# Performance work log

Measured on AMD Instinct MI355X. Metric: run time of the kernel, lower is better.

Reference implementation:

```python
import jax, jax.numpy as jnp
import numpy as np

SEQ_LEN = 512
PRED_LEN = 96
N_BINS = 5


def setup_inputs() -> dict:
    key = jax.random.key(0)
    k1, k2, k3 = jax.random.split(key, 3)
    x = jax.random.normal(k1, (64, 1024, SEQ_LEN), dtype=jnp.float32)
    # nn.Linear(seq_len, pred_len): weight (pred_len, seq_len), bias (pred_len,)
    W = jax.random.normal(k2, (PRED_LEN, SEQ_LEN), dtype=jnp.float32) / np.sqrt(SEQ_LEN)
    b = jax.random.normal(k3, (PRED_LEN,), dtype=jnp.float32) * 0.01
    return {"x": x, "W": W, "b": b}


def reference(x, W, b):
    # Exact low-pass trend: keep lowest N_BINS rfft bins, zero the rest, invert.
    X = jnp.fft.rfft(x, axis=-1)                      # (B, N, seq_len//2+1) complex
    n_freq = X.shape[-1]
    keep = (jnp.arange(n_freq) < N_BINS)              # low-pass mask
    X_low = jnp.where(keep, X, 0.0)
    trend = jnp.fft.irfft(X_low, n=SEQ_LEN, axis=-1).astype(x.dtype)  # (B, N, seq_len)
    resid = x - trend
    trend_forecast = jnp.einsum('bns,ps->bnp', trend, W) + b          # (B, N, pred_len)
    return (trend_forecast, resid)
```

## Files before the change

### kernel.cpp

```cpp
#include <hip/hip_runtime.h>

#define SEQL 512
#define PREDL 96
#define NB 9
#define WBPAD 12
#define RU 4

typedef float fvec4 __attribute__((ext_vector_type(4)));

static __device__ __constant__ double TWO_PI_OVER_S = 6.283185307179586476925286766559 / (double)SEQL;

__device__ __forceinline__ float wave_sum_bcast(float v) {
    int t;
    t = __builtin_amdgcn_update_dpp(0, __float_as_int(v), 0x111, 0xf, 0xf, true); v += __int_as_float(t);
    t = __builtin_amdgcn_update_dpp(0, __float_as_int(v), 0x112, 0xf, 0xf, true); v += __int_as_float(t);
    t = __builtin_amdgcn_update_dpp(0, __float_as_int(v), 0x114, 0xf, 0xf, true); v += __int_as_float(t);
    t = __builtin_amdgcn_update_dpp(0, __float_as_int(v), 0x118, 0xf, 0xf, true); v += __int_as_float(t);
    t = __builtin_amdgcn_update_dpp(0, __float_as_int(v), 0x142, 0xf, 0xf, true); v += __int_as_float(t);
    t = __builtin_amdgcn_update_dpp(0, __float_as_int(v), 0x143, 0xf, 0xf, true); v += __int_as_float(t);
    return __int_as_float(__builtin_amdgcn_readlane(__float_as_int(v), 63));
}

__global__ void basis_kernel(float* __restrict__ tbl) {
    int s = threadIdx.x;
    if (s >= SEQL) return;
    tbl[0 * SEQL + s] = 1.0f;
    #pragma unroll
    for (int k = 1; k <= 4; ++k) {
        double ang = TWO_PI_OVER_S * (double)(k * s);
        tbl[(2 * k - 1) * SEQL + s] = (float)cos(ang);
        tbl[(2 * k    ) * SEQL + s] = (float)sin(ang);
    }
}

__global__ __launch_bounds__(64)
void wb_kernel(const float* __restrict__ W, const float* __restrict__ tbl,
               float* __restrict__ wb) {
    int p = blockIdx.x;
    int lane = threadIdx.x;
    const float* wr = W + (size_t)p * SEQL + lane * 8;
    float4 wa = *(const float4*)(wr);
    float4 wz = *(const float4*)(wr + 4);
    float wv[8] = {wa.x, wa.y, wa.z, wa.w, wz.x, wz.y, wz.z, wz.w};
    #pragma unroll
    for (int j = 0; j < NB; ++j) {
        const float* bj = tbl + j * SEQL + lane * 8;
        float4 b0 = *(const float4*)bj;
        float4 b1 = *(const float4*)(bj + 4);
        float bb[8] = {b0.x, b0.y, b0.z, b0.w, b1.x, b1.y, b1.z, b1.w};
        float acc = 0.f;
        #pragma unroll
        for (int e = 0; e < 8; ++e) acc += wv[e] * bb[e];
        float s = wave_sum_bcast(acc);
        if (lane == 0) wb[p * WBPAD + j] = s;
    }
}

__global__ __launch_bounds__(256)
void detrend_kernel(const float* __restrict__ x, const float* __restrict__ bias,
                    const float* __restrict__ tbl, const float* __restrict__ wb,
                    float* __restrict__ fc, float* __restrict__ resid, int nrows) {
    const int lane = threadIdx.x & 63;
    const int wid  = threadIdx.x >> 6;
    const int wpb  = blockDim.x >> 6;
    const int gw   = blockIdx.x * wpb + wid;
    const int nw   = gridDim.x * wpb;

    float bas[NB][8];
    #pragma unroll
    for (int j = 0; j < NB; ++j) {
        const float* bj = tbl + j * SEQL + lane * 8;
        float4 b0 = *(const float4*)bj;
        float4 b1 = *(const float4*)(bj + 4);
        bas[j][0] = b0.x; bas[j][1] = b0.y; bas[j][2] = b0.z; bas[j][3] = b0.w;
        bas[j][4] = b1.x; bas[j][5] = b1.y; bas[j][6] = b1.z; bas[j][7] = b1.w;
    }
    const int p0 = lane;
    const int p1 = 64 + lane;
    float wb0[NB], wb1[NB], bv0, bv1 = 0.f;
    #pragma unroll
    for (int j = 0; j < NB; ++j) wb0[j] = wb[p0 * WBPAD + j];
    bv0 = bias[p0];
    if (lane < 32) {
        #pragma unroll
        for (int j = 0; j < NB; ++j) wb1[j] = wb[p1 * WBPAD + j];
        bv1 = bias[p1];
    }

    for (int r0 = gw * RU; r0 < nrows; r0 += nw * RU) {
        float xv[RU][8];
        #pragma unroll
        for (int u = 0; u < RU; ++u) {
            const float* xr = x + (size_t)(r0 + u) * SEQL + lane * 8;
            float4 xa = *(const float4*)xr;
            float4 xb = *(const float4*)(xr + 4);
            xv[u][0] = xa.x; xv[u][1] = xa.y; xv[u][2] = xa.z; xv[u][3] = xa.w;
            xv[u][4] = xb.x; xv[u][5] = xb.y; xv[u][6] = xb.z; xv[u][7] = xb.w;
        }

        float c[RU][NB];
        #pragma unroll
        for (int u = 0; u < RU; ++u) {
            float acc[NB];
            #pragma unroll
            for (int j = 0; j < NB; ++j) acc[j] = 0.f;
            #pragma unroll
            for (int e = 0; e < 8; ++e)
                #pragma unroll
                for (int j = 0; j < NB; ++j) acc[j] += xv[u][e] * bas[j][e];
            acc[0] *= (1.0f / SEQL);
            #pragma unroll
            for (int j = 1; j < NB; ++j) acc[j] *= (2.0f / SEQL);
            #pragma unroll
            for (int j = 0; j < NB; ++j) c[u][j] = wave_sum_bcast(acc[j]);
        }

        #pragma unroll
        for (int u = 0; u < RU; ++u) {
            float rv[8];
            #pragma unroll
            for (int e = 0; e < 8; ++e) {
                float t = 0.f;
                #pragma unroll
                for (int j = 0; j < NB; ++j) t += c[u][j] * bas[j][e];
                rv[e] = xv[u][e] - t;
            }
            float* rr = resid + (size_t)(r0 + u) * SEQL + lane * 8;
            fvec4 v0 = {rv[0], rv[1], rv[2], rv[3]};
            fvec4 v1 = {rv[4], rv[5], rv[6], rv[7]};
            __builtin_nontemporal_store(v0, (fvec4*)rr);
            __builtin_nontemporal_store(v1, (fvec4*)(rr + 4));
        }

        #pragma unroll
        for (int u = 0; u < RU; ++u) {
            float* fr = fc + (size_t)(r0 + u) * PREDL;
            float f0 = bv0;
            #pragma unroll
            for (int j = 0; j < NB; ++j) f0 += c[u][j] * wb0[j];
            __builtin_nontemporal_store(f0, fr + p0);
            if (lane < 32) {
                float f1 = bv1;
                #pragma unroll
                for (int j = 0; j < NB; ++j) f1 += c[u][j] * wb1[j];
                __builtin_nontemporal_store(f1, fr + p1);
            }
        }
    }
}

extern "C" void kernel_launch(void* const* d_in, const int* in_sizes, int n_in,
                              void* d_out, int out_size, void* d_ws, size_t ws_size,
                              hipStream_t stream) {
    const float* x = (const float*)d_in[0];
    const float* W = (const float*)d_in[1];
    const float* b = (const float*)d_in[2];
    float* fc = (float*)d_out;
    const int nrows = in_sizes[0] / SEQL;
    float* resid = fc + (size_t)nrows * PREDL;
    float* tbl = (float*)d_ws;
    float* wb  = tbl + NB * SEQL;

    hipLaunchKernelGGL(basis_kernel, dim3(1), dim3(SEQL), 0, stream, tbl);
    hipLaunchKernelGGL(wb_kernel, dim3(PREDL), dim3(64), 0, stream, W, tbl, wb);
    hipLaunchKernelGGL(detrend_kernel, dim3(2048), dim3(256), 0, stream,
                       x, b, tbl, wb, fc, resid, nrows);
}
```

Baseline: 64.87 us.

## Issue all row loads upfront with one tile per wave and fast basis sincos

```diff
diff --git a/kernel.cpp b/kernel.cpp
--- a/kernel.cpp
+++ b/kernel.cpp
@@ -4,11 +4,9 @@
 #define PREDL 96
 #define NB 9
 #define WBPAD 12
-#define RU 4
+#define RU 8
 
 typedef float fvec4 __attribute__((ext_vector_type(4)));
-
-static __device__ __constant__ double TWO_PI_OVER_S = 6.283185307179586476925286766559 / (double)SEQL;
 
 __device__ __forceinline__ float wave_sum_bcast(float v) {
     int t;
@@ -27,9 +25,12 @@
     tbl[0 * SEQL + s] = 1.0f;
     #pragma unroll
     for (int k = 1; k <= 4; ++k) {
-        double ang = TWO_PI_OVER_S * (double)(k * s);
-        tbl[(2 * k - 1) * SEQL + s] = (float)cos(ang);
-        tbl[(2 * k    ) * SEQL + s] = (float)sin(ang);
+        int m = (k * s) & (SEQL - 1);
+        float ang = (float)m * (6.283185307179586f / SEQL);
+        float sn, cs;
+        __sincosf(ang, &sn, &cs);
+        tbl[(2 * k - 1) * SEQL + s] = cs;
+        tbl[(2 * k    ) * SEQL + s] = sn;
     }
 }
 
@@ -56,15 +57,23 @@
     }
 }
 
-__global__ __launch_bounds__(256)
+__global__ __launch_bounds__(256, 2)
 void detrend_kernel(const float* __restrict__ x, const float* __restrict__ bias,
                     const float* __restrict__ tbl, const float* __restrict__ wb,
                     float* __restrict__ fc, float* __restrict__ resid, int nrows) {
     const int lane = threadIdx.x & 63;
     const int wid  = threadIdx.x >> 6;
-    const int wpb  = blockDim.x >> 6;
-    const int gw   = blockIdx.x * wpb + wid;
-    const int nw   = gridDim.x * wpb;
+    const int gw   = blockIdx.x * (blockDim.x >> 6) + wid;
+    const int r0   = gw * RU;
+    if (r0 >= nrows) return;
+
+    float4 xl[RU][2];
+    #pragma unroll
+    for (int u = 0; u < RU; ++u) {
+        const float* xr = x + (size_t)(r0 + u) * SEQL + lane * 8;
+        xl[u][0] = *(const float4*)xr;
+        xl[u][1] = *(const float4*)(xr + 4);
+    }
 
     float bas[NB][8];
     #pragma unroll
@@ -87,64 +96,48 @@
         bv1 = bias[p1];
     }
 
-    for (int r0 = gw * RU; r0 < nrows; r0 += nw * RU) {
-        float xv[RU][8];
+    #pragma unroll
+    for (int u = 0; u < RU; ++u) {
+        float xv[8] = {xl[u][0].x, xl[u][0].y, xl[u][0].z, xl[u][0].w,
+                       xl[u][1].x, xl[u][1].y, xl[u][1].z, xl[u][1].w};
+        float acc[NB];
         #pragma unroll
-        for (int u = 0; u < RU; ++u) {
-            const float* xr = x + (size_t)(r0 + u) * SEQL + lane * 8;
-            float4 xa = *(const float4*)xr;
-            float4 xb = *(const float4*)(xr + 4);
-            xv[u][0] = xa.x; xv[u][1] = xa.y; xv[u][2] = xa.z; xv[u][3] = xa.w;
-            xv[u][4] = xb.x; xv[u][5] = xb.y; xv[u][6] = xb.z; xv[u][7] = xb.w;
+        for (int j = 0; j < NB; ++j) acc[j] = 0.f;
+        #pragma unroll
+        for (int e = 0; e < 8; ++e)
+            #pragma unroll
+            for (int j = 0; j < NB; ++j) acc[j] += xv[e] * bas[j][e];
+        acc[0] *= (1.0f / SEQL);
+        #pragma unroll
+        for (int j = 1; j < NB; ++j) acc[j] *= (2.0f / SEQL);
+        float c[NB];
+        #pragma unroll
+        for (int j = 0; j < NB; ++j) c[j] = wave_sum_bcast(acc[j]);
+
+        float rv[8];
+        #pragma unroll
+        for (int e = 0; e < 8; ++e) {
+            float t = 0.f;
+            #pragma unroll
+            for (int j = 0; j < NB; ++j) t += c[j] * bas[j][e];
+            rv[e] = xv[e] - t;
         }
+        float* rr = resid + (size_t)(r0 + u) * SEQL + lane * 8;
+        fvec4 v0 = {rv[0], rv[1], rv[2], rv[3]};
+        fvec4 v1 = {rv[4], rv[5], rv[6], rv[7]};
+        __builtin_nontemporal_store(v0, (fvec4*)rr);
+        __builtin_nontemporal_store(v1, (fvec4*)(rr + 4));
 
-        float c[RU][NB];
+        float* fr = fc + (size_t)(r0 + u) * PREDL;
+        float f0 = bv0;
         #pragma unroll
-        for (int u = 0; u < RU; ++u) {
-            float acc[NB];
+        for (int j = 0; j < NB; ++j) f0 += c[j] * wb0[j];
+        __builtin_nontemporal_store(f0, fr + p0);
+        if (lane < 32) {
+            float f1 = bv1;
             #pragma unroll
-            for (int j = 0; j < NB; ++j) acc[j] = 0.f;
-            #pragma unroll
-            for (int e = 0; e < 8; ++e)
-                #pragma unroll
-                for (int j = 0; j < NB; ++j) acc[j] += xv[u][e] * bas[j][e];
-            acc[0] *= (1.0f / SEQL);
-            #pragma unroll
-            for (int j = 1; j < NB; ++j) acc[j] *= (2.0f / SEQL);
-            #pragma unroll
-            for (int j = 0; j < NB; ++j) c[u][j] = wave_sum_bcast(acc[j]);
-        }
-
-        #pragma unroll
-        for (int u = 0; u < RU; ++u) {
-            float rv[8];
-            #pragma unroll
-            for (int e = 0; e < 8; ++e) {
-                float t = 0.f;
-                #pragma unroll
-                for (int j = 0; j < NB; ++j) t += c[u][j] * bas[j][e];
-                rv[e] = xv[u][e] - t;
-            }
-            float* rr = resid + (size_t)(r0 + u) * SEQL + lane * 8;
-            fvec4 v0 = {rv[0], rv[1], rv[2], rv[3]};
-            fvec4 v1 = {rv[4], rv[5], rv[6], rv[7]};
-            __builtin_nontemporal_store(v0, (fvec4*)rr);
-            __builtin_nontemporal_store(v1, (fvec4*)(rr + 4));
-        }
-
-        #pragma unroll
-        for (int u = 0; u < RU; ++u) {
-            float* fr = fc + (size_t)(r0 + u) * PREDL;
-            float f0 = bv0;
-            #pragma unroll
-            for (int j = 0; j < NB; ++j) f0 += c[u][j] * wb0[j];
-            __builtin_nontemporal_store(f0, fr + p0);
-            if (lane < 32) {
-                float f1 = bv1;
-                #pragma unroll
-                for (int j = 0; j < NB; ++j) f1 += c[u][j] * wb1[j];
-                __builtin_nontemporal_store(f1, fr + p1);
-            }
+            for (int j = 0; j < NB; ++j) f1 += c[j] * wb1[j];
+            __builtin_nontemporal_store(f1, fr + p1);
         }
     }
 }
```

Result: slower. 67.83 us (+4.6%).
